# Kernel optimization log

Measured on AMD Instinct MI355X. Metric: run time of the kernel, lower is better.

Reference implementation:

```python
import jax, jax.numpy as jnp
import numpy as np

EPS = 1e-6

def elu_plus_one(x):
    # F.elu(x) + 1 == exp(x) for x<=0, x+1 for x>0
    return jnp.where(x > 0, x + 1.0, jnp.exp(jnp.minimum(x, 0.0)))

def setup_inputs() -> dict:
    key = jax.random.key(0)
    k1, k2, k3, k4, k5 = jax.random.split(key, 5)
    B, S, D, M = 2, 4096, 1024, 4
    queries = jax.random.normal(k1, (B, S, D), dtype=jnp.float32)
    keys = jax.random.normal(k2, (B, S, D), dtype=jnp.float32)
    values = jax.random.normal(k3, (B, S, D), dtype=jnp.float32)
    # small-scale warm memory state; norms positive (accumulated sigma(k) sums)
    memories = jax.random.normal(k4, (M, D, D), dtype=jnp.float32) * 0.02
    memory_norms = jax.random.uniform(k5, (M, D), dtype=jnp.float32)
    return {"queries": queries, "keys": keys, "values": values,
            "memories": memories, "memory_norms": memory_norms}

def reference(queries, keys, values, memories, memory_norms):
    B, S, D = queries.shape
    M = memories.shape[0]

    # ---------------- retrieve ----------------
    sigma_q = elu_plus_one(queries)                                   # (B,S,D)
    a_mem = jnp.einsum('bsd,mde->mbse', sigma_q, memories)            # (M,B,S,D)
    qnorm = jnp.einsum('bsd,md->mbs', sigma_q, memory_norms)          # (M,B,S)
    outputs = a_mem / jnp.clip(qnorm, EPS, None)[..., None]           # (M,B,S,D)
    # relevance: sigma(Q) @ landmark, mean over seq -> (M,B)
    rel = qnorm.mean(axis=-1)
    empty = jnp.sum(jnp.abs(memory_norms), axis=1) < EPS              # (M,)
    NEG = jnp.float32(-1e30)
    rel = jnp.where(empty[:, None], NEG, rel)
    weights = jax.nn.softmax(rel, axis=0)                             # (M,B)
    outputs = jnp.where(empty[:, None, None, None], 0.0, outputs)
    out = jnp.einsum('mbsd,mb->bsd', outputs, weights)
    # if every slot empty, torch returns zeros
    out = jnp.where(jnp.all(empty), jnp.zeros_like(out), out)

    # ---------------- update (delta rule, current_idx = 0) ----------------
    sigma_k = elu_plus_one(keys)                                      # (B,S,D)
    mem0, norm0 = memories[0], memory_norms[0]
    retrieved_unnorm = jnp.matmul(sigma_k, mem0)                      # (B,S,D)
    knorm = jnp.clip(jnp.matmul(sigma_k, norm0), EPS, None)[..., None]
    delta_v = values - retrieved_unnorm / knorm
    mem_update = jnp.einsum('bsd,bse->de', sigma_k, delta_v) / (B * S)
    new_memory = jax.lax.stop_gradient(mem0 + mem_update)             # .detach()
    new_memory_norm = jax.lax.stop_gradient(norm0 + sigma_k.sum(axis=(0, 1)) / B)
    return out, new_memory, new_memory_norm
```

## Files before the change

### kernel.cpp

```cpp
#include <hip/hip_runtime.h>
#include <math.h>

#define B_ 2
#define S_ 4096
#define D_ 1024
#define M_ 4
#define N_ (B_*S_)
#define EPS 1e-6f

typedef unsigned short u16;
typedef __bf16 bf16x8 __attribute__((ext_vector_type(8)));
typedef float  f32x4  __attribute__((ext_vector_type(4)));

__device__ __forceinline__ float elu1(float x) {
    return x > 0.0f ? x + 1.0f : __expf(x);
}

__device__ __forceinline__ u16 f2b(float f) {
    unsigned int u = __float_as_uint(f);
    return (u16)((u + 0x7FFFu + ((u >> 16) & 1u)) >> 16);
}

#define GLDS16(gp, lp) __builtin_amdgcn_global_load_lds( \
    (const __attribute__((address_space(1))) void*)(gp), \
    (__attribute__((address_space(3))) void*)(lp), 16, 0, 0)

__global__ __launch_bounds__(256) void zero_small(float* knorm, float* colsum) {
    int t = blockIdx.x * 256 + threadIdx.x;
    if (t < N_) knorm[t] = 0.0f;
    if (t < D_) colsum[t] = 0.0f;
}

__global__ __launch_bounds__(256) void k1_stats(
    const float* __restrict__ Q, const float* __restrict__ mnorm,
    float* __restrict__ qnorm,
    u16* __restrict__ sQ)
{
    int r = blockIdx.x;
    int t = threadIdx.x;
    float4 q4 = *(const float4*)(Q + (size_t)r * D_ + t * 4);
    float sq0 = elu1(q4.x), sq1 = elu1(q4.y), sq2 = elu1(q4.z), sq3 = elu1(q4.w);

    uint2 sv;
    sv.x = (unsigned)f2b(sq0) | ((unsigned)f2b(sq1) << 16);
    sv.y = (unsigned)f2b(sq2) | ((unsigned)f2b(sq3) << 16);
    *(uint2*)(sQ + (size_t)r * D_ + t * 4) = sv;

    float vals[M_];
    #pragma unroll
    for (int m = 0; m < M_; ++m) {
        float4 w4 = *(const float4*)(mnorm + m * D_ + t * 4);
        vals[m] = sq0 * w4.x + sq1 * w4.y + sq2 * w4.z + sq3 * w4.w;
    }

    __shared__ float sbuf[M_][4];
    int wave = t >> 6, lane = t & 63;
    #pragma unroll
    for (int i = 0; i < M_; ++i) {
        float v = vals[i];
        #pragma unroll
        for (int off = 32; off > 0; off >>= 1) v += __shfl_down(v, off, 64);
        if (lane == 0) sbuf[i][wave] = v;
    }
    __syncthreads();
    if (t == 0) {
        #pragma unroll
        for (int m = 0; m < M_; ++m)
            qnorm[(size_t)m * N_ + r] = sbuf[m][0] + sbuf[m][1] + sbuf[m][2] + sbuf[m][3];
    }
}

__global__ __launch_bounds__(256) void prep_k(
    const float* __restrict__ K, const float* __restrict__ mnorm,
    u16* __restrict__ sk, u16* __restrict__ skT,
    float* __restrict__ colsum, float* __restrict__ knorm)
{
    __shared__ float tile[64][65];
    __shared__ float mn0[64];
    int r0 = blockIdx.x * 64;
    int d0 = blockIdx.y * 64;
    int t = threadIdx.x;
    int rr = t >> 4, c4 = (t & 15) * 4;
    if (t >= 128 && t < 192) mn0[t - 128] = mnorm[d0 + (t - 128)];
    #pragma unroll
    for (int i = 0; i < 4; ++i) {
        int rri = rr + i * 16;
        float4 k4 = *(const float4*)(K + (size_t)(r0 + rri) * D_ + d0 + c4);
        float e0 = elu1(k4.x), e1 = elu1(k4.y), e2 = elu1(k4.z), e3 = elu1(k4.w);
        uint2 v; v.x = (unsigned)f2b(e0) | ((unsigned)f2b(e1) << 16);
        v.y = (unsigned)f2b(e2) | ((unsigned)f2b(e3) << 16);
        *(uint2*)(sk + (size_t)(r0 + rri) * D_ + d0 + c4) = v;
        tile[rri][c4 + 0] = e0; tile[rri][c4 + 1] = e1;
        tile[rri][c4 + 2] = e2; tile[rri][c4 + 3] = e3;
    }
    __syncthreads();
    #pragma unroll
    for (int i = 0; i < 4; ++i) {
        int dd = rr + i * 16;
        float v0 = tile[c4 + 0][dd], v1 = tile[c4 + 1][dd];
        float v2 = tile[c4 + 2][dd], v3 = tile[c4 + 3][dd];
        uint2 v; v.x = (unsigned)f2b(v0) | ((unsigned)f2b(v1) << 16);
        v.y = (unsigned)f2b(v2) | ((unsigned)f2b(v3) << 16);
        *(uint2*)(skT + (size_t)(d0 + dd) * N_ + r0 + c4) = v;
    }
    if (t < 64) {
        float s = 0.0f;
        #pragma unroll
        for (int j = 0; j < 64; ++j) s += tile[t][j] * mn0[j];
        atomicAdd(&knorm[r0 + t], s);
    } else if (t < 128) {
        int c = t - 64;
        float s = 0.0f;
        #pragma unroll
        for (int j = 0; j < 64; ++j) s += tile[j][c];
        atomicAdd(&colsum[d0 + c], s);
    }
}

__global__ __launch_bounds__(256) void prep_memT(
    const float* __restrict__ Mem, u16* __restrict__ MemT)
{
    __shared__ float tile[64][65];
    int m = blockIdx.z;
    int e0 = blockIdx.x * 64, d0 = blockIdx.y * 64;
    int t = threadIdx.x, rr = t >> 4, c4 = (t & 15) * 4;
    #pragma unroll
    for (int i = 0; i < 4; ++i) {
        int dd = rr + i * 16;
        float4 v4 = *(const float4*)(Mem + ((size_t)m * D_ + d0 + dd) * D_ + e0 + c4);
        tile[dd][c4 + 0] = v4.x; tile[dd][c4 + 1] = v4.y;
        tile[dd][c4 + 2] = v4.z; tile[dd][c4 + 3] = v4.w;
    }
    __syncthreads();
    #pragma unroll
    for (int i = 0; i < 4; ++i) {
        int ee = rr + i * 16;
        float v0 = tile[c4 + 0][ee], v1 = tile[c4 + 1][ee];
        float v2 = tile[c4 + 2][ee], v3 = tile[c4 + 3][ee];
        uint2 v; v.x = (unsigned)f2b(v0) | ((unsigned)f2b(v1) << 16);
        v.y = (unsigned)f2b(v2) | ((unsigned)f2b(v3) << 16);
        *(uint2*)(MemT + (size_t)(e0 + ee) * (M_ * D_) + m * D_ + d0 + c4) = v;
    }
}

__global__ __launch_bounds__(256) void k2_weights(
    const float* __restrict__ mnorm, const float* __restrict__ qnorm,
    float* __restrict__ weights)
{
    __shared__ float sbuf[12][4];
    int t = threadIdx.x, wave = t >> 6, lane = t & 63;
    float vals[12];
    #pragma unroll
    for (int m = 0; m < M_; ++m) {
        float v = 0.0f;
        for (int d = t; d < D_; d += 256) v += fabsf(mnorm[m * D_ + d]);
        vals[m] = v;
    }
    #pragma unroll
    for (int mb = 0; mb < M_ * B_; ++mb) {
        int m = mb >> 1, b = mb & 1;
        const float4* p = (const float4*)(qnorm + (size_t)m * N_ + (size_t)b * S_);
        float v = 0.0f;
        for (int i = t; i < S_ / 4; i += 256) {
            float4 x = p[i];
            v += x.x + x.y + x.z + x.w;
        }
        vals[4 + mb] = v;
    }
    #pragma unroll
    for (int i = 0; i < 12; ++i) {
        float v = vals[i];
        #pragma unroll
        for (int off = 32; off > 0; off >>= 1) v += __shfl_down(v, off, 64);
        if (lane == 0) sbuf[i][wave] = v;
    }
    __syncthreads();
    if (t == 0) {
        bool empty[M_]; bool all_empty = true;
        float relsum[M_ * B_];
        #pragma unroll
        for (int m = 0; m < M_; ++m) {
            float sa = sbuf[m][0] + sbuf[m][1] + sbuf[m][2] + sbuf[m][3];
            empty[m] = (sa < EPS);
            all_empty = all_empty && empty[m];
        }
        #pragma unroll
        for (int mb = 0; mb < M_ * B_; ++mb)
            relsum[mb] = sbuf[4 + mb][0] + sbuf[4 + mb][1] + sbuf[4 + mb][2] + sbuf[4 + mb][3];
        for (int b = 0; b < B_; ++b) {
            float rel[M_]; float mx = -3.0e38f;
            #pragma unroll
            for (int m = 0; m < M_; ++m) {
                rel[m] = empty[m] ? -1.0e30f : relsum[m * B_ + b] * (1.0f / (float)S_);
                mx = fmaxf(mx, rel[m]);
            }
            float se = 0.0f;
            #pragma unroll
            for (int m = 0; m < M_; ++m) { rel[m] = __expf(rel[m] - mx); se += rel[m]; }
            #pragma unroll
            for (int m = 0; m < M_; ++m) {
                float wv = rel[m] / se;
                if (empty[m] || all_empty) wv = 0.0f;
                weights[m * B_ + b] = wv;
            }
        }
    }
}

__global__ __launch_bounds__(256) void k2_cvec(
    const float* __restrict__ qnorm, const float* __restrict__ weights,
    const float* __restrict__ mnorm, const float* __restrict__ colsum,
    float* __restrict__ ratT, float* __restrict__ norm_out)
{
    int g = blockIdx.x * 256 + threadIdx.x;
    if (g < N_) {
        int b = g / S_;
        float cs[M_];
        #pragma unroll
        for (int m = 0; m < M_; ++m)
            cs[m] = fmaxf(weights[m * B_ + b] / fmaxf(qnorm[(size_t)m * N_ + g], EPS), 1e-20f);
        ratT[0 * (size_t)N_ + g] = cs[0] / cs[1];
        ratT[1 * (size_t)N_ + g] = cs[1] / cs[2];
        ratT[2 * (size_t)N_ + g] = cs[2] / cs[3];
        ratT[3 * (size_t)N_ + g] = cs[3];
    }
    if (g < D_) norm_out[g] = mnorm[g] + colsum[g] * (1.0f / (float)B_);
}

__global__ __launch_bounds__(256) void k_copy_mem(
    const float* __restrict__ mem, float* __restrict__ dst)
{
    int g = blockIdx.x * 256 + threadIdx.x;
    float4 v = *(const float4*)(mem + (size_t)g * 4);
    *(float4*)(dst + (size_t)g * 4) = v;
}

__device__ __forceinline__ void tile_mma(
    const u16* Asb, const u16* Bsb, int aoff, int boff, f32x4 (&acc)[4][4])
{
    bf16x8 af[4], bf[4];
    #pragma unroll
    for (int i = 0; i < 4; ++i) {
        af[i] = *(const bf16x8*)((const char*)Asb + aoff + i * 1024);
        bf[i] = *(const bf16x8*)((const char*)Bsb + boff + i * 1024);
    }
    #pragma unroll
    for (int mi = 0; mi < 4; ++mi)
        #pragma unroll
        for (int ni = 0; ni < 4; ++ni)
            acc[mi][ni] = __builtin_amdgcn_mfma_f32_16x16x32_bf16(
                af[mi], bf[ni], acc[mi][ni], 0, 0, 0);
}

__device__ __forceinline__ void gemm_seg(
    u16* As, u16* Bs,
    const u16* __restrict__ A, int lda, int ak0,
    const u16* __restrict__ B, int ldb, int bk0,
    int rb, int cb, int klen,
    f32x4 (&acc)[4][4])
{
    const int tid  = threadIdx.x;
    const int lane = tid & 63;
    const int wid  = tid >> 6;
    const int wr   = wid >> 1, wc = wid & 1;
    const int r15  = lane & 15;

    const int srow0 = (wid * 2 + 0) * 16 + (lane >> 2);
    const int srow1 = (wid * 2 + 1) * 16 + (lane >> 2);
    const int sg    = ((lane & 3) ^ ((lane >> 3) & 3)) * 8;
    const u16* Ag0 = A + (size_t)(rb + srow0) * lda + ak0 + sg;
    const u16* Ag1 = A + (size_t)(rb + srow1) * lda + ak0 + sg;
    const u16* Bg0 = B + (size_t)(cb + srow0) * ldb + bk0 + sg;
    const u16* Bg1 = B + (size_t)(cb + srow1) * ldb + bk0 + sg;
    const int lo0 = (wid * 2 + 0) * 512;
    const int lo1 = (wid * 2 + 1) * 512;

    const int xo   = (((lane >> 4) ^ ((r15 >> 1) & 3)) * 16);
    const int aoff = (wr * 64 + r15) * 64 + xo;
    const int boff = (wc * 64 + r15) * 64 + xo;

    GLDS16(Ag0, As + lo0);
    GLDS16(Ag1, As + lo1);
    GLDS16(Bg0, Bs + lo0);
    GLDS16(Bg1, Bs + lo1);
    asm volatile("s_waitcnt vmcnt(0)" ::: "memory");
    __builtin_amdgcn_s_barrier();

    int cur = 0;
    for (int kt = 32; kt < klen; kt += 32) {
        int nxt = cur ^ 1;
        GLDS16(Ag0 + kt, As + nxt * 4096 + lo0);
        GLDS16(Ag1 + kt, As + nxt * 4096 + lo1);
        GLDS16(Bg0 + kt, Bs + nxt * 4096 + lo0);
        GLDS16(Bg1 + kt, Bs + nxt * 4096 + lo1);
        tile_mma(As + cur * 4096, Bs + cur * 4096, aoff, boff, acc);
        asm volatile("s_waitcnt vmcnt(0) lgkmcnt(0)" ::: "memory");
        __builtin_amdgcn_s_barrier();
        cur = nxt;
    }
    tile_mma(As + cur * 4096, Bs + cur * 4096, aoff, boff, acc);
    asm volatile("s_waitcnt lgkmcnt(0)" ::: "memory");
    __builtin_amdgcn_s_barrier();
}

__device__ __forceinline__ void epi_out(
    f32x4 (&acc)[4][4], float* __restrict__ out, int rb, int cb)
{
    int lane = threadIdx.x & 63, wid = threadIdx.x >> 6;
    int wr = wid >> 1, wc = wid & 1, r15 = lane & 15;
    #pragma unroll
    for (int mi = 0; mi < 4; ++mi) {
        int row0 = rb + wr * 64 + mi * 16 + (lane >> 4) * 4;
        #pragma unroll
        for (int ni = 0; ni < 4; ++ni) {
            int col = cb + wc * 64 + ni * 16 + r15;
            #pragma unroll
            for (int r = 0; r < 4; ++r)
                out[(size_t)(row0 + r) * D_ + col] = acc[mi][ni][r];
        }
    }
}

__device__ __forceinline__ void epi_delta(
    f32x4 (&acc)[4][4], const float* __restrict__ V,
    const float* __restrict__ knorm, u16* __restrict__ deltaT,
    int rb, int cb)
{
    int lane = threadIdx.x & 63, wid = threadIdx.x >> 6;
    int wr = wid >> 1, wc = wid & 1, r15 = lane & 15;
    #pragma unroll
    for (int mi = 0; mi < 4; ++mi) {
        int row0 = rb + wr * 64 + mi * 16 + (lane >> 4) * 4;
        float inv[4];
        #pragma unroll
        for (int r = 0; r < 4; ++r) inv[r] = 1.0f / fmaxf(knorm[row0 + r], EPS);
        #pragma unroll
        for (int ni = 0; ni < 4; ++ni) {
            int col = cb + wc * 64 + ni * 16 + r15;
            float dv[4];
            #pragma unroll
            for (int r = 0; r < 4; ++r)
                dv[r] = V[(size_t)(row0 + r) * D_ + col] - acc[mi][ni][r] * inv[r];
            uint2 pv;
            pv.x = (unsigned)f2b(dv[0]) | ((unsigned)f2b(dv[1]) << 16);
            pv.y = (unsigned)f2b(dv[2]) | ((unsigned)f2b(dv[3]) << 16);
            *(uint2*)(deltaT + (size_t)col * N_ + row0) = pv;
        }
    }
}

__global__ __launch_bounds__(256, 4) void g34_fused(
    const u16* __restrict__ sQ, const u16* __restrict__ MemT,
    const u16* __restrict__ sk, const float* __restrict__ V,
    const float* __restrict__ knorm, const float* __restrict__ ratT,
    float* __restrict__ out, u16* __restrict__ deltaT)
{
    __shared__ u16 As[2 * 4096];
    __shared__ u16 Bs[2 * 4096];
    int hw = blockIdx.x;
    int x  = hw & 7;
    int l  = hw >> 3;
    int z  = l >> 6;
    int by = l & 63, bx = x;
    int rb = by * 128, cb = bx * 128;
    int lane = threadIdx.x & 63, wid = threadIdx.x >> 6;
    int wr = wid >> 1;
    f32x4 acc[4][4];
    #pragma unroll
    for (int i = 0; i < 4; ++i)
        #pragma unroll
        for (int j = 0; j < 4; ++j) {
            f32x4 zz = {0.0f, 0.0f, 0.0f, 0.0f};
            acc[i][j] = zz;
        }
    if (z == 0) {
        #pragma unroll 1
        for (int m = 0; m < M_; ++m) {
            gemm_seg(As, Bs, sQ, D_, 0, MemT, M_ * D_, m * D_, rb, cb, D_, acc);
            const float* rp = ratT + (size_t)m * N_;
            #pragma unroll
            for (int mi = 0; mi < 4; ++mi) {
                int row0 = rb + wr * 64 + mi * 16 + (lane >> 4) * 4;
                float4 rt = *(const float4*)(rp + row0);
                #pragma unroll
                for (int ni = 0; ni < 4; ++ni) {
                    acc[mi][ni][0] *= rt.x; acc[mi][ni][1] *= rt.y;
                    acc[mi][ni][2] *= rt.z; acc[mi][ni][3] *= rt.w;
                }
            }
        }
        epi_out(acc, out, rb, cb);
    } else {
        gemm_seg(As, Bs, sk, D_, 0, MemT, M_ * D_, 0, rb, cb, D_, acc);
        epi_delta(acc, V, knorm, deltaT, rb, cb);
    }
}

#define KSPLIT 8
__global__ __launch_bounds__(256, 4) void g5_update(
    const u16* __restrict__ skT, const u16* __restrict__ deltaT,
    float* __restrict__ memout)
{
    __shared__ u16 As[2 * 4096];
    __shared__ u16 Bs[2 * 4096];
    f32x4 acc[4][4];
    #pragma unroll
    for (int i = 0; i < 4; ++i)
        #pragma unroll
        for (int j = 0; j < 4; ++j) {
            f32x4 zz = {0.0f, 0.0f, 0.0f, 0.0f};
            acc[i][j] = zz;
        }
    int rb = blockIdx.y * 128, cb = blockIdx.x * 128;
    int k0 = blockIdx.z * (N_ / KSPLIT);
    gemm_seg(As, Bs, skT, N_, k0, deltaT, N_, k0, rb, cb, N_ / KSPLIT, acc);
    int lane = threadIdx.x & 63, wid = threadIdx.x >> 6;
    int wr = wid >> 1, wc = wid & 1, r15 = lane & 15;
    const float sc = 1.0f / (float)N_;
    #pragma unroll
    for (int mi = 0; mi < 4; ++mi) {
        int row0 = rb + wr * 64 + mi * 16 + (lane >> 4) * 4;
        #pragma unroll
        for (int ni = 0; ni < 4; ++ni) {
            int col = cb + wc * 64 + ni * 16 + r15;
            #pragma unroll
            for (int r = 0; r < 4; ++r)
                atomicAdd(memout + (size_t)(row0 + r) * D_ + col, acc[mi][ni][r] * sc);
        }
    }
}

extern "C" void kernel_launch(void* const* d_in, const int* in_sizes, int n_in,
                              void* d_out, int out_size, void* d_ws, size_t ws_size,
                              hipStream_t stream) {
    const float* Q     = (const float*)d_in[0];
    const float* K     = (const float*)d_in[1];
    const float* V     = (const float*)d_in[2];
    const float* Mem   = (const float*)d_in[3];
    const float* Mnorm = (const float*)d_in[4];

    float* out      = (float*)d_out;
    float* out_mem  = out + (size_t)N_ * D_;
    float* out_norm = out_mem + (size_t)D_ * D_;

    char* wsb = (char*)d_ws;
    float* qnorm   = (float*)wsb;
    float* knorm   = qnorm + (size_t)M_ * N_;
    float* colsum  = knorm + N_;
    float* weights = colsum + D_;
    float* ratT    = weights + M_ * B_;
    u16* MemT   = (u16*)(wsb + (size_t)1  * (1 << 20));
    u16* sk     = (u16*)(wsb + (size_t)9  * (1 << 20));
    u16* skT    = (u16*)(wsb + (size_t)25 * (1 << 20));
    u16* sQ     = (u16*)(wsb + (size_t)41 * (1 << 20));
    u16* deltaT = (u16*)(wsb + (size_t)57 * (1 << 20));

    hipLaunchKernelGGL(zero_small, dim3(32), dim3(256), 0, stream, knorm, colsum);
    hipLaunchKernelGGL(k1_stats, dim3(N_), dim3(256), 0, stream, Q, Mnorm, qnorm, sQ);
    hipLaunchKernelGGL(prep_k, dim3(128, 16), dim3(256), 0, stream, K, Mnorm, sk, skT, colsum, knorm);
    hipLaunchKernelGGL(prep_memT, dim3(16, 16, 4), dim3(256), 0, stream, Mem, MemT);
    hipLaunchKernelGGL(k2_weights, dim3(1), dim3(256), 0, stream, Mnorm, qnorm, weights);
    hipLaunchKernelGGL(k2_cvec, dim3(32), dim3(256), 0, stream, qnorm, weights, Mnorm, colsum, ratT, out_norm);
    hipLaunchKernelGGL(k_copy_mem, dim3((D_ * D_ / 4) / 256), dim3(256), 0, stream, Mem, out_mem);
    hipLaunchKernelGGL(g34_fused, dim3(1024), dim3(256), 0, stream,
                       sQ, MemT, sk, V, knorm, ratT, out, deltaT);
    hipLaunchKernelGGL(g5_update, dim3(8, 8, KSPLIT), dim3(256), 0, stream, skT, deltaT, out_mem);
}
```

Before: 231.8 us.

## Split memory-slot loop across two blocks per tile and combine via atomics

The retrieve GEMM previously ran all four memory slots sequentially in one block per output tile. It now splits them into two pairs handled by separate blocks, which combine their partial results into a pre-zeroed output using float atomicAdd. The ratio vector is adjusted so each pair's chained scaling stays correct. This raises grid size and parallelism (occupancy hint raised to 5) to balance against the delta blocks, at the cost of an extra zeroing pass over the output and atomic read-modify-write traffic.

New measurement: 300.4 us. +29.6%, slower.

```diff
diff --git a/kernel.cpp b/kernel.cpp
--- a/kernel.cpp
+++ b/kernel.cpp
@@ -29,6 +29,12 @@
     int t = blockIdx.x * 256 + threadIdx.x;
     if (t < N_) knorm[t] = 0.0f;
     if (t < D_) colsum[t] = 0.0f;
+}
+
+__global__ __launch_bounds__(256) void zero_out(float* out) {
+    size_t g = (size_t)blockIdx.x * 256 + threadIdx.x;
+    float4 z = make_float4(0.f, 0.f, 0.f, 0.f);
+    *(float4*)(out + g * 4) = z;
 }
 
 __global__ __launch_bounds__(256) void k1_stats(
@@ -220,7 +226,7 @@
         for (int m = 0; m < M_; ++m)
             cs[m] = fmaxf(weights[m * B_ + b] / fmaxf(qnorm[(size_t)m * N_ + g], EPS), 1e-20f);
         ratT[0 * (size_t)N_ + g] = cs[0] / cs[1];
-        ratT[1 * (size_t)N_ + g] = cs[1] / cs[2];
+        ratT[1 * (size_t)N_ + g] = cs[1];
         ratT[2 * (size_t)N_ + g] = cs[2] / cs[3];
         ratT[3 * (size_t)N_ + g] = cs[3];
     }
@@ -303,24 +309,6 @@
     __builtin_amdgcn_s_barrier();
 }
 
-__device__ __forceinline__ void epi_out(
-    f32x4 (&acc)[4][4], float* __restrict__ out, int rb, int cb)
-{
-    int lane = threadIdx.x & 63, wid = threadIdx.x >> 6;
-    int wr = wid >> 1, wc = wid & 1, r15 = lane & 15;
-    #pragma unroll
-    for (int mi = 0; mi < 4; ++mi) {
-        int row0 = rb + wr * 64 + mi * 16 + (lane >> 4) * 4;
-        #pragma unroll
-        for (int ni = 0; ni < 4; ++ni) {
-            int col = cb + wc * 64 + ni * 16 + r15;
-            #pragma unroll
-            for (int r = 0; r < 4; ++r)
-                out[(size_t)(row0 + r) * D_ + col] = acc[mi][ni][r];
-        }
-    }
-}
-
 __device__ __forceinline__ void epi_delta(
     f32x4 (&acc)[4][4], const float* __restrict__ V,
     const float* __restrict__ knorm, u16* __restrict__ deltaT,
@@ -349,7 +337,7 @@
     }
 }
 
-__global__ __launch_bounds__(256, 4) void g34_fused(
+__global__ __launch_bounds__(256, 5) void g34_fused(
     const u16* __restrict__ sQ, const u16* __restrict__ MemT,
     const u16* __restrict__ sk, const float* __restrict__ V,
     const float* __restrict__ knorm, const float* __restrict__ ratT,
@@ -358,13 +346,8 @@
     __shared__ u16 As[2 * 4096];
     __shared__ u16 Bs[2 * 4096];
     int hw = blockIdx.x;
-    int x  = hw & 7;
-    int l  = hw >> 3;
-    int z  = l >> 6;
-    int by = l & 63, bx = x;
-    int rb = by * 128, cb = bx * 128;
     int lane = threadIdx.x & 63, wid = threadIdx.x >> 6;
-    int wr = wid >> 1;
+    int wr = wid >> 1, wc = wid & 1, r15 = lane & 15;
     f32x4 acc[4][4];
     #pragma unroll
     for (int i = 0; i < 4; ++i)
@@ -373,24 +356,41 @@
             f32x4 zz = {0.0f, 0.0f, 0.0f, 0.0f};
             acc[i][j] = zz;
         }
-    if (z == 0) {
-        #pragma unroll 1
-        for (int m = 0; m < M_; ++m) {
-            gemm_seg(As, Bs, sQ, D_, 0, MemT, M_ * D_, m * D_, rb, cb, D_, acc);
-            const float* rp = ratT + (size_t)m * N_;
-            #pragma unroll
-            for (int mi = 0; mi < 4; ++mi) {
-                int row0 = rb + wr * 64 + mi * 16 + (lane >> 4) * 4;
-                float4 rt = *(const float4*)(rp + row0);
+    if (hw < 1024) {
+        int bx = hw & 7, by = (hw >> 3) & 63, mp = hw >> 9;
+        int rb = by * 128, cb = bx * 128;
+        int m0 = mp * 2;
+        const float* rat = ratT + (size_t)(2 * mp) * N_;
+        const float* scl = ratT + (size_t)(2 * mp + 1) * N_;
+        gemm_seg(As, Bs, sQ, D_, 0, MemT, M_ * D_, m0 * D_, rb, cb, D_, acc);
+        #pragma unroll
+        for (int mi = 0; mi < 4; ++mi) {
+            int row0 = rb + wr * 64 + mi * 16 + (lane >> 4) * 4;
+            float4 rt = *(const float4*)(rat + row0);
+            #pragma unroll
+            for (int ni = 0; ni < 4; ++ni) {
+                acc[mi][ni][0] *= rt.x; acc[mi][ni][1] *= rt.y;
+                acc[mi][ni][2] *= rt.z; acc[mi][ni][3] *= rt.w;
+            }
+        }
+        gemm_seg(As, Bs, sQ, D_, 0, MemT, M_ * D_, (m0 + 1) * D_, rb, cb, D_, acc);
+        #pragma unroll
+        for (int mi = 0; mi < 4; ++mi) {
+            int row0 = rb + wr * 64 + mi * 16 + (lane >> 4) * 4;
+            float4 sc4 = *(const float4*)(scl + row0);
+            float scv[4] = {sc4.x, sc4.y, sc4.z, sc4.w};
+            #pragma unroll
+            for (int ni = 0; ni < 4; ++ni) {
+                int col = cb + wc * 64 + ni * 16 + r15;
                 #pragma unroll
-                for (int ni = 0; ni < 4; ++ni) {
-                    acc[mi][ni][0] *= rt.x; acc[mi][ni][1] *= rt.y;
-                    acc[mi][ni][2] *= rt.z; acc[mi][ni][3] *= rt.w;
-                }
+                for (int r = 0; r < 4; ++r)
+                    atomicAdd(out + (size_t)(row0 + r) * D_ + col, acc[mi][ni][r] * scv[r]);
             }
         }
-        epi_out(acc, out, rb, cb);
     } else {
+        int d = hw - 1024;
+        int bx = d & 7, by = d >> 3;
+        int rb = by * 128, cb = bx * 128;
         gemm_seg(As, Bs, sk, D_, 0, MemT, M_ * D_, 0, rb, cb, D_, acc);
         epi_delta(acc, V, knorm, deltaT, rb, cb);
     }
@@ -456,13 +456,14 @@
     u16* deltaT = (u16*)(wsb + (size_t)57 * (1 << 20));
 
     hipLaunchKernelGGL(zero_small, dim3(32), dim3(256), 0, stream, knorm, colsum);
+    hipLaunchKernelGGL(zero_out, dim3((N_ * (D_ / 4)) / 256), dim3(256), 0, stream, out);
     hipLaunchKernelGGL(k1_stats, dim3(N_), dim3(256), 0, stream, Q, Mnorm, qnorm, sQ);
     hipLaunchKernelGGL(prep_k, dim3(128, 16), dim3(256), 0, stream, K, Mnorm, sk, skT, colsum, knorm);
     hipLaunchKernelGGL(prep_memT, dim3(16, 16, 4), dim3(256), 0, stream, Mem, MemT);
     hipLaunchKernelGGL(k2_weights, dim3(1), dim3(256), 0, stream, Mnorm, qnorm, weights);
     hipLaunchKernelGGL(k2_cvec, dim3(32), dim3(256), 0, stream, qnorm, weights, Mnorm, colsum, ratT, out_norm);
     hipLaunchKernelGGL(k_copy_mem, dim3((D_ * D_ / 4) / 256), dim3(256), 0, stream, Mem, out_mem);
-    hipLaunchKernelGGL(g34_fused, dim3(1024), dim3(256), 0, stream,
+    hipLaunchKernelGGL(g34_fused, dim3(1536), dim3(256), 0, stream,
                        sQ, MemT, sk, V, knorm, ratT, out, deltaT);
     hipLaunchKernelGGL(g5_update, dim3(8, 8, KSPLIT), dim3(256), 0, stream, skT, deltaT, out_mem);
 }
```
